# Optimization experiments

Measured on AMD Instinct MI355X. Metric: run time of the kernel, lower is better.

## Reference

```python
import jax, jax.numpy as jnp
import numpy as np

B, IN, OUT, TDIM, YDIM = 4096, 48, 64, 128, 64
HID = OUT * OUT  # 4096, Y_layer hidden/output width


def setup_inputs() -> dict:
    key = jax.random.key(0)
    ks = jax.random.split(key, 9)
    x = jax.random.normal(ks[0], (B, IN, IN), dtype=jnp.float32)
    # symmetrize so input is SPD-like (module assumes SPD inputs)
    x = 0.5 * (x + jnp.swapaxes(x, 1, 2))
    t = jax.random.normal(ks[1], (B, TDIM), dtype=jnp.float32)
    Y = jax.random.normal(ks[2], (B, YDIM), dtype=jnp.float32)
    # Stiefel (orthogonal) weight [input_size(=OUT after increase), output_size]
    W, _ = jnp.linalg.qr(jax.random.normal(ks[3], (OUT, OUT), dtype=jnp.float32))
    # Y_layer MLP params: Linear(YDIM,HID) -> SiLU -> Linear(HID,HID)
    Y_W1 = jax.random.normal(ks[4], (YDIM, HID), dtype=jnp.float32) / np.sqrt(YDIM)
    Y_b1 = jnp.zeros((HID,), dtype=jnp.float32)
    Y_W2 = jax.random.normal(ks[5], (HID, HID), dtype=jnp.float32) / np.sqrt(HID)
    Y_b2 = jnp.zeros((HID,), dtype=jnp.float32)
    return {"input": x, "t": t, "Y": Y, "W": W,
            "Y_W1": Y_W1, "Y_b1": Y_b1, "Y_W2": Y_W2, "Y_b2": Y_b2}


def reference(input, t, Y, W, Y_W1, Y_b1, Y_W2, Y_b2):
    # Y_layer MLP -> per-sample transform emb_Y [B, OUT, OUT]
    h = jax.nn.silu(Y @ Y_W1 + Y_b1)
    emb_Y = (h @ Y_W2 + Y_b2).reshape(B, OUT, OUT)
    # SPDIncreaseDim: embed input in top-left of OUTxOUT, ones on padded diagonal
    pad = OUT - IN
    xp = jnp.pad(input, ((0, 0), (0, pad), (0, pad)))
    add_diag = jnp.concatenate([jnp.zeros(IN, input.dtype), jnp.ones(pad, input.dtype)])
    xp = xp + jnp.diag(add_diag)[None]
    # congruence with Stiefel weight: W^T X W
    out = jnp.einsum('ji,bjk,kl->bil', W, xp, W)
    # congruence with MLP-generated weight: emb_Y X emb_Y^T
    out = jnp.einsum('bij,bjk,blk->bil', emb_Y, out, emb_Y)
    return out
```

## Files before the change

### kernel.cpp

```cpp
#include <hip/hip_runtime.h>
#include <hip/hip_bf16.h>

typedef __bf16 bf16;
typedef __bf16 bf16x8 __attribute__((ext_vector_type(8)));
typedef float floatx4 __attribute__((ext_vector_type(4)));

#define MFMA16(a, b, c) __builtin_amdgcn_mfma_f32_16x16x32_bf16((a), (b), (c), 0, 0, 0)

__device__ inline void gload_lds16(const void* g, void* l) {
    __builtin_amdgcn_global_load_lds((__attribute__((address_space(1))) void*)g,
                                     (__attribute__((address_space(3))) void*)l, 16, 0, 0);
}

__global__ __launch_bounds__(256) void prep_fused(
    const float* __restrict__ W2,
    const float* __restrict__ W,
    const float* __restrict__ b2,
    const float* __restrict__ Y,
    const float* __restrict__ W1,
    const float* __restrict__ b1,
    bf16* __restrict__ W2fT,
    float* __restrict__ b2f,
    bf16* __restrict__ h)
{
    __shared__ __align__(16) char smem[45056];
    int t = threadIdx.x, bid = blockIdx.x;
    int w = t >> 6, l = t & 63;
    int lm = l & 15, q2 = l >> 4, q8 = q2 * 8;

    if (bid < 2048) {
        int pt = bid & 31, i = bid >> 5;
        bf16* sW = (bf16*)smem;
        bf16* sA = sW + 64 * 72;
        bf16* sT = sA + 128 * 72;
        int p0 = pt * 128;

#pragma unroll
        for (int kk = 0; kk < 4; kk++) {
            int idx4 = t + 256 * kk;
            float4 v = *(const float4*)(W + (size_t)idx4 * 4);
            int row = (idx4 * 4) >> 6, col = (idx4 * 4) & 63;
            bf16 tmp[4] = {(bf16)v.x, (bf16)v.y, (bf16)v.z, (bf16)v.w};
            *(uint2*)(sW + row * 72 + col) = *(const uint2*)tmp;
        }
        {
            const float* src = W2 + (size_t)p0 * 4096 + i * 64;
#pragma unroll
            for (int kk = 0; kk < 8; kk++) {
                int c = t + 256 * kk;
                int row = c >> 4, j4 = (c & 15) * 4;
                float4 v = *(const float4*)(src + (size_t)row * 4096 + j4);
                bf16 tmp[4] = {(bf16)v.x, (bf16)v.y, (bf16)v.z, (bf16)v.w};
                *(uint2*)(sA + row * 72 + j4) = *(const uint2*)tmp;
            }
        }
        __syncthreads();

        floatx4 acc[2][4] = {};
#pragma unroll
        for (int kc = 0; kc < 2; kc++) {
            bf16x8 a0 = *(const bf16x8*)(sA + (w * 32 + lm) * 72 + kc * 32 + q8);
            bf16x8 a1 = *(const bf16x8*)(sA + (w * 32 + 16 + lm) * 72 + kc * 32 + q8);
#pragma unroll
            for (int jn = 0; jn < 4; jn++) {
                bf16x8 bf_ = *(const bf16x8*)(sW + (jn * 16 + lm) * 72 + kc * 32 + q8);
                acc[0][jn] = MFMA16(a0, bf_, acc[0][jn]);
                acc[1][jn] = MFMA16(a1, bf_, acc[1][jn]);
            }
        }
#pragma unroll
        for (int im = 0; im < 2; im++)
#pragma unroll
            for (int jn = 0; jn < 4; jn++) {
                int pr = w * 32 + im * 16 + q2 * 4;
                int lc = jn * 16 + lm;
                union { bf16 h4[4]; uint2 u; } pk;
#pragma unroll
                for (int r = 0; r < 4; r++) pk.h4[r] = (bf16)acc[im][jn][r];
                *(uint2*)(sT + lc * 136 + pr) = pk.u;
            }
        __syncthreads();
#pragma unroll
        for (int kk = 0; kk < 4; kk++) {
            int c = t + 256 * kk;
            int row = c >> 4, off = (c & 15) * 8;
            uint4 v = *(const uint4*)(sT + row * 136 + off);
            *(uint4*)(W2fT + (size_t)(i * 64 + row) * 4096 + p0 + off) = v;
        }
        return;
    }

    if (bid < 2112) {
        int i = bid - 2048;
        if (t < 64) {
            float acc = 0.f;
            const float* b2r = b2 + i * 64;
            const float* wr_ = W + t * 64;
#pragma unroll
            for (int j = 0; j < 64; j++) acc = fmaf(b2r[j], wr_[j], acc);
            b2f[i * 64 + t] = acc;
        }
        return;
    }

    {
        int q = bid - 2112;
        int m0 = (q >> 5) * 128, n0 = (q & 31) * 128;
        bf16* sY = (bf16*)smem;
        bf16* sWT = sY + 128 * 72;

#pragma unroll
        for (int kk = 0; kk < 8; kk++) {
            int c = t + 256 * kk;
            int row = c >> 4, c4 = (c & 15) * 4;
            float4 v = *(const float4*)(Y + (size_t)(m0 + row) * 64 + c4);
            bf16 tmp[4] = {(bf16)v.x, (bf16)v.y, (bf16)v.z, (bf16)v.w};
            *(uint2*)(sY + row * 72 + c4) = *(const uint2*)tmp;
        }
#pragma unroll
        for (int kk = 0; kk < 8; kk++) {
            int c = t + 256 * kk;
            int k = c >> 5, j4 = (c & 31) * 4;
            float4 v = *(const float4*)(W1 + (size_t)k * 4096 + n0 + j4);
            sWT[(j4 + 0) * 72 + k] = (bf16)v.x;
            sWT[(j4 + 1) * 72 + k] = (bf16)v.y;
            sWT[(j4 + 2) * 72 + k] = (bf16)v.z;
            sWT[(j4 + 3) * 72 + k] = (bf16)v.w;
        }
        __syncthreads();

        int wn = (w & 1) * 64, wm = (w >> 1) * 64;
        floatx4 acc[4][4] = {};
#pragma unroll
        for (int kc = 0; kc < 2; kc++) {
            bf16x8 af[4], bfr[4];
#pragma unroll
            for (int i = 0; i < 4; i++)
                af[i] = *(const bf16x8*)(sWT + (wn + i * 16 + lm) * 72 + kc * 32 + q8);
#pragma unroll
            for (int j = 0; j < 4; j++)
                bfr[j] = *(const bf16x8*)(sY + (wm + j * 16 + lm) * 72 + kc * 32 + q8);
#pragma unroll
            for (int i = 0; i < 4; i++)
#pragma unroll
                for (int j = 0; j < 4; j++)
                    acc[i][j] = MFMA16(af[i], bfr[j], acc[i][j]);
        }
#pragma unroll
        for (int i = 0; i < 4; i++) {
            int nb = n0 + wn + i * 16 + q2 * 4;
            float4 bv = *(const float4*)(b1 + nb);
            float bb[4] = {bv.x, bv.y, bv.z, bv.w};
#pragma unroll
            for (int j = 0; j < 4; j++) {
                int m = m0 + wm + j * 16 + lm;
                union { bf16 h4[4]; uint2 u; } pk;
#pragma unroll
                for (int r = 0; r < 4; r++) {
                    float v = acc[i][j][r] + bb[r];
                    v = v / (1.f + __expf(-v));
                    pk.h4[r] = (bf16)v;
                }
                *(uint2*)(h + (size_t)m * 4096 + nb) = pk.u;
            }
        }
    }
}

__global__ __launch_bounds__(512, 2) void gemm_bt_bias(
    const bf16* __restrict__ A, const bf16* __restrict__ BT,
    const float* __restrict__ bias, bf16* __restrict__ C,
    int M, int N, int K)
{
    __shared__ __align__(16) char lds[131072];

    int t = threadIdx.x, w = t >> 6, l = t & 63;
    int lm = l & 15, q2 = l >> 4;
    int wm = w >> 2, wn = w & 3;

    int bid = blockIdx.x;
    int xcd = bid & 7, local = bid >> 3;
    int m0 = ((xcd & 3) * 4 + (local >> 3)) * 256;
    int n0 = ((xcd >> 2) * 8 + (local & 7)) * 256;

    int c1 = t + 512;
    int ks0 = ((t & 3) ^ ((t >> 3) & 3)) * 8;
    int ks1 = ((c1 & 3) ^ ((c1 >> 3) & 3)) * 8;
    const bf16* gA0 = A + (size_t)(m0 + (t >> 2)) * K + ks0;
    const bf16* gA1 = A + (size_t)(m0 + (c1 >> 2)) * K + ks1;
    const bf16* gB0 = BT + (size_t)(n0 + (t >> 2)) * K + ks0;
    const bf16* gB1 = BT + (size_t)(n0 + (c1 >> 2)) * K + ks1;
    const int dst0 = (w * 64) * 16, dst1 = (512 + w * 64) * 16;

    auto issueA = [&](int slot) {
        char* slab = lds + slot * 32768;
        gload_lds16(gA0, slab + dst0);
        gload_lds16(gA1, slab + dst1);
        gA0 += 32; gA1 += 32;
    };
    auto issueB = [&](int slot) {
        char* slab = lds + slot * 32768;
        gload_lds16(gB0, slab + 16384 + dst0);
        gload_lds16(gB1, slab + 16384 + dst1);
        gB0 += 32; gB1 += 32;
    };

    const int qp16 = (q2 ^ ((lm >> 1) & 3)) * 16;
    const int aoff = (wm * 128 + lm) * 64 + qp16;
    const int boff = 16384 + (wn * 64 + lm) * 64 + qp16;

    floatx4 acc[8][4] = {};

    auto body = [&](int kt, bool doIssue) {
        const char* slab = lds + (kt & 3) * 32768;
        int s = (kt + 3) & 3;
        bf16x8 bv[4], a0[4], a1[4];
#pragma unroll
        for (int j = 0; j < 4; j++) bv[j] = *(const bf16x8*)(slab + boff + j * 1024);
#pragma unroll
        for (int i = 0; i < 4; i++) a0[i] = *(const bf16x8*)(slab + aoff + i * 1024);
        __builtin_amdgcn_sched_barrier(0);
#pragma unroll
        for (int i = 0; i < 4; i++) a1[i] = *(const bf16x8*)(slab + aoff + (4 + i) * 1024);
        if (doIssue) { issueA(s); issueB(s); }
        asm volatile("s_waitcnt lgkmcnt(4)" ::: "memory");
        __builtin_amdgcn_sched_barrier(0);
        __builtin_amdgcn_s_setprio(1);
#pragma unroll
        for (int i = 0; i < 4; i++)
#pragma unroll
            for (int j = 0; j < 4; j++) acc[i][j] = MFMA16(bv[j], a0[i], acc[i][j]);
        __builtin_amdgcn_s_setprio(0);
        asm volatile("s_waitcnt lgkmcnt(0)" ::: "memory");
        __builtin_amdgcn_sched_barrier(0);
        __builtin_amdgcn_s_setprio(1);
#pragma unroll
        for (int i = 0; i < 4; i++)
#pragma unroll
            for (int j = 0; j < 4; j++) acc[4 + i][j] = MFMA16(bv[j], a1[i], acc[4 + i][j]);
        __builtin_amdgcn_s_setprio(0);
        __builtin_amdgcn_sched_barrier(0);
    };

    issueA(0); issueB(0); issueA(1); issueB(1); issueA(2); issueB(2);
    asm volatile("s_waitcnt vmcnt(8)" ::: "memory");
    __builtin_amdgcn_s_barrier();
    const int KT = K >> 5;
    for (int kt = 0; kt < KT - 3; ++kt) {
        body(kt, true);
        asm volatile("s_waitcnt vmcnt(8)" ::: "memory");
        __builtin_amdgcn_s_barrier();
    }
    body(KT - 3, false);
    asm volatile("s_waitcnt vmcnt(4)" ::: "memory");
    __builtin_amdgcn_s_barrier();
    body(KT - 2, false);
    asm volatile("s_waitcnt vmcnt(0)" ::: "memory");
    __builtin_amdgcn_s_barrier();
    body(KT - 1, false);

#pragma unroll
    for (int i = 0; i < 8; i++) {
        int m = m0 + wm * 128 + i * 16 + lm;
#pragma unroll
        for (int j = 0; j < 4; j++) {
            int nb = n0 + wn * 64 + j * 16 + q2 * 4;
            float4 b4 = *(const float4*)(bias + nb);
            float bb[4] = {b4.x, b4.y, b4.z, b4.w};
            union { bf16 h4[4]; uint2 u; } pk;
#pragma unroll
            for (int r = 0; r < 4; r++) pk.h4[r] = (bf16)(acc[i][j][r] + bb[r]);
            *(uint2*)(C + (size_t)m * N + nb) = pk.u;
        }
    }
}

#define ST 72
__global__ __launch_bounds__(256) void batched_congruence(
    const float* __restrict__ x,
    const bf16* __restrict__ F,
    float* __restrict__ out)
{
    __shared__ bf16 sX[64 * ST], sF[64 * ST], sT[64 * ST];
    int t = threadIdx.x, w = t >> 6, l = t & 63;
    int b = blockIdx.x;
    int lm = l & 15, q2 = l >> 4, q8 = q2 * 8;
    int r0 = (w >> 1) * 32, c0 = (w & 1) * 32;

    const float4* xb = (const float4*)(x + (size_t)b * 2304);
    float4 v0 = xb[t];
    float4 v1 = xb[t + 256];
    float4 v2 = (t < 64) ? xb[t + 512] : make_float4(0.f, 0.f, 0.f, 0.f);

    {
        const uint4* gf = (const uint4*)(F + (size_t)b * 4096);
#pragma unroll
        for (int kk = 0; kk < 2; kk++) {
            int c = t + 256 * kk;
            *(uint4*)(sF + (c >> 3) * ST + (c & 7) * 8) = gf[c];
        }
    }
    {
        unsigned* sx32 = (unsigned*)sX;
#pragma unroll
        for (int kk = 0; kk < 4; kk++) {
            int idx = t + 256 * kk;
            if (idx < 384) {
                int r = idx >> 3, d = 24 + (idx & 7);
                sx32[r * 36 + d] = 0u;
            } else if (idx < 896) {
                int k2 = idx - 384;
                int r = 48 + (k2 >> 5), d = k2 & 31;
                unsigned val = 0u;
                if (d == (r >> 1)) val = (r & 1) ? 0x3F800000u : 0x00003F80u;
                sx32[r * 36 + d] = val;
            }
        }
    }
    {
        int c = t;
        bf16 p4[4];
        p4[0] = (bf16)v0.x; p4[1] = (bf16)v0.y; p4[2] = (bf16)v0.z; p4[3] = (bf16)v0.w;
        *(uint2*)(sX + (c / 12) * ST + (c % 12) * 4) = *(const uint2*)p4;
        c = t + 256;
        p4[0] = (bf16)v1.x; p4[1] = (bf16)v1.y; p4[2] = (bf16)v1.z; p4[3] = (bf16)v1.w;
        *(uint2*)(sX + (c / 12) * ST + (c % 12) * 4) = *(const uint2*)p4;
        if (t < 64) {
            c = t + 512;
            p4[0] = (bf16)v2.x; p4[1] = (bf16)v2.y; p4[2] = (bf16)v2.z; p4[3] = (bf16)v2.w;
            *(uint2*)(sX + (c / 12) * ST + (c % 12) * 4) = *(const uint2*)p4;
        }
    }
    __syncthreads();

    auto mm = [&](const bf16* PA, const bf16* PB, floatx4 acc[2][2]) {
#pragma unroll
        for (int kc = 0; kc < 2; kc++) {
            bf16x8 a0 = *(const bf16x8*)(PA + (r0 + lm) * ST + kc * 32 + q8);
            bf16x8 a1 = *(const bf16x8*)(PA + (r0 + 16 + lm) * ST + kc * 32 + q8);
            bf16x8 b0 = *(const bf16x8*)(PB + (c0 + lm) * ST + kc * 32 + q8);
            bf16x8 b1 = *(const bf16x8*)(PB + (c0 + 16 + lm) * ST + kc * 32 + q8);
            acc[0][0] = MFMA16(a0, b0, acc[0][0]);
            acc[0][1] = MFMA16(a0, b1, acc[0][1]);
            acc[1][0] = MFMA16(a1, b0, acc[1][0]);
            acc[1][1] = MFMA16(a1, b1, acc[1][1]);
        }
    };

    floatx4 z = {0.f, 0.f, 0.f, 0.f};
    {
        floatx4 acc[2][2] = {{z, z}, {z, z}};
        mm(sX, sF, acc);
#pragma unroll
        for (int i = 0; i < 2; i++)
#pragma unroll
            for (int j = 0; j < 2; j++) {
                int R = r0 + i * 16 + q2 * 4;
                int Cc = c0 + j * 16 + lm;
                union { bf16 h4[4]; uint2 u; } pk;
#pragma unroll
                for (int r = 0; r < 4; r++) pk.h4[r] = (bf16)acc[i][j][r];
                *(uint2*)(sT + Cc * ST + R) = pk.u;
            }
    }
    __syncthreads();
    {
        floatx4 acc[2][2] = {{z, z}, {z, z}};
        mm(sT, sF, acc);
        float* stage = (float*)sX;
        float* ob = out + (size_t)b * 4096;
        if (w < 2) {
#pragma unroll
            for (int i = 0; i < 2; i++)
#pragma unroll
                for (int j = 0; j < 2; j++) {
                    int R = r0 + i * 16 + q2 * 4;
                    int Cc = c0 + j * 16 + lm;
#pragma unroll
                    for (int r = 0; r < 4; r++) stage[(R + r) * 64 + Cc] = acc[i][j][r];
                }
        }
        __syncthreads();
#pragma unroll
        for (int kk = 0; kk < 2; kk++) {
            int idx = t + 256 * kk;
            *(float4*)(ob + (size_t)idx * 4) = *(const float4*)(stage + (size_t)idx * 4);
        }
        __syncthreads();
        if (w >= 2) {
#pragma unroll
            for (int i = 0; i < 2; i++)
#pragma unroll
                for (int j = 0; j < 2; j++) {
                    int R = r0 + i * 16 + q2 * 4 - 32;
                    int Cc = c0 + j * 16 + lm;
#pragma unroll
                    for (int r = 0; r < 4; r++) stage[(R + r) * 64 + Cc] = acc[i][j][r];
                }
        }
        __syncthreads();
#pragma unroll
        for (int kk = 0; kk < 2; kk++) {
            int idx = t + 256 * kk;
            *(float4*)(ob + 2048 + (size_t)idx * 4) = *(const float4*)(stage + (size_t)idx * 4);
        }
    }
}

extern "C" void kernel_launch(void* const* d_in, const int* in_sizes, int n_in,
                              void* d_out, int out_size, void* d_ws, size_t ws_size,
                              hipStream_t stream) {
    const float* x  = (const float*)d_in[0];
    const float* Y  = (const float*)d_in[2];
    const float* W  = (const float*)d_in[3];
    const float* W1 = (const float*)d_in[4];
    const float* b1 = (const float*)d_in[5];
    const float* W2 = (const float*)d_in[6];
    const float* b2 = (const float*)d_in[7];
    float* out = (float*)d_out;

    const size_t NN = (size_t)4096 * 4096;
    bf16* h    = (bf16*)d_ws;
    bf16* W2fT = h + NN;
    bf16* emb  = W2fT + NN;
    float* b2f = (float*)d_out;

    prep_fused<<<3136, 256, 0, stream>>>(W2, W, b2, Y, W1, b1, W2fT, b2f, h);
    gemm_bt_bias<<<256, 512, 0, stream>>>(h, W2fT, b2f, emb, 4096, 4096, 4096);
    batched_congruence<<<4096, 256, 0, stream>>>(x, emb, out);
}
```

Before: 307.5 us.

## Switch GEMM pipeline to double-buffered BK=64 slabs with one barrier per step

```diff
diff --git a/kernel.cpp b/kernel.cpp
--- a/kernel.cpp
+++ b/kernel.cpp
@@ -183,46 +183,51 @@
     int m0 = ((xcd & 3) * 4 + (local >> 3)) * 256;
     int n0 = ((xcd >> 2) * 8 + (local & 7)) * 256;
 
-    int c1 = t + 512;
-    int ks0 = ((t & 3) ^ ((t >> 3) & 3)) * 8;
-    int ks1 = ((c1 & 3) ^ ((c1 >> 3) & 3)) * 8;
-    const bf16* gA0 = A + (size_t)(m0 + (t >> 2)) * K + ks0;
-    const bf16* gA1 = A + (size_t)(m0 + (c1 >> 2)) * K + ks1;
-    const bf16* gB0 = BT + (size_t)(n0 + (t >> 2)) * K + ks0;
-    const bf16* gB1 = BT + (size_t)(n0 + (c1 >> 2)) * K + ks1;
-    const int dst0 = (w * 64) * 16, dst1 = (512 + w * 64) * 16;
-
-    auto issueA = [&](int slot) {
-        char* slab = lds + slot * 32768;
-        gload_lds16(gA0, slab + dst0);
-        gload_lds16(gA1, slab + dst1);
-        gA0 += 32; gA1 += 32;
+    const bf16 *gA0, *gA1, *gA2, *gA3, *gB0, *gB1, *gB2, *gB3;
+    {
+        int ch, row, ko;
+        ch = t;        row = ch >> 3; ko = ((ch & 7) ^ (row & 7)) * 8;
+        gA0 = A + (size_t)(m0 + row) * K + ko; gB0 = BT + (size_t)(n0 + row) * K + ko;
+        ch = t + 512;  row = ch >> 3; ko = ((ch & 7) ^ (row & 7)) * 8;
+        gA1 = A + (size_t)(m0 + row) * K + ko; gB1 = BT + (size_t)(n0 + row) * K + ko;
+        ch = t + 1024; row = ch >> 3; ko = ((ch & 7) ^ (row & 7)) * 8;
+        gA2 = A + (size_t)(m0 + row) * K + ko; gB2 = BT + (size_t)(n0 + row) * K + ko;
+        ch = t + 1536; row = ch >> 3; ko = ((ch & 7) ^ (row & 7)) * 8;
+        gA3 = A + (size_t)(m0 + row) * K + ko; gB3 = BT + (size_t)(n0 + row) * K + ko;
+    }
+    const int dstb = t * 16;
+
+    auto issue = [&](int slot) {
+        char* slab = lds + (slot << 16);
+        gload_lds16(gA0, slab + dstb);
+        gload_lds16(gA1, slab + 8192 + dstb);
+        gload_lds16(gA2, slab + 16384 + dstb);
+        gload_lds16(gA3, slab + 24576 + dstb);
+        gload_lds16(gB0, slab + 32768 + dstb);
+        gload_lds16(gB1, slab + 40960 + dstb);
+        gload_lds16(gB2, slab + 49152 + dstb);
+        gload_lds16(gB3, slab + 57344 + dstb);
+        gA0 += 64; gA1 += 64; gA2 += 64; gA3 += 64;
+        gB0 += 64; gB1 += 64; gB2 += 64; gB3 += 64;
     };
-    auto issueB = [&](int slot) {
-        char* slab = lds + slot * 32768;
-        gload_lds16(gB0, slab + 16384 + dst0);
-        gload_lds16(gB1, slab + 16384 + dst1);
-        gB0 += 32; gB1 += 32;
-    };
-
-    const int qp16 = (q2 ^ ((lm >> 1) & 3)) * 16;
-    const int aoff = (wm * 128 + lm) * 64 + qp16;
-    const int boff = 16384 + (wn * 64 + lm) * 64 + qp16;
+
+    const int swz = (q2 ^ (lm & 7)) * 16;
+    const int base_a = (wm * 128 + lm) * 128 + swz;
+    const int base_b = 32768 + (wn * 64 + lm) * 128 + swz;
 
     floatx4 acc[8][4] = {};
 
     auto body = [&](int kt, bool doIssue) {
-        const char* slab = lds + (kt & 3) * 32768;
-        int s = (kt + 3) & 3;
+        const char* slab = lds + ((kt & 1) << 16);
         bf16x8 bv[4], a0[4], a1[4];
 #pragma unroll
-        for (int j = 0; j < 4; j++) bv[j] = *(const bf16x8*)(slab + boff + j * 1024);
-#pragma unroll
-        for (int i = 0; i < 4; i++) a0[i] = *(const bf16x8*)(slab + aoff + i * 1024);
-        __builtin_amdgcn_sched_barrier(0);
-#pragma unroll
-        for (int i = 0; i < 4; i++) a1[i] = *(const bf16x8*)(slab + aoff + (4 + i) * 1024);
-        if (doIssue) { issueA(s); issueB(s); }
+        for (int j = 0; j < 4; j++) bv[j] = *(const bf16x8*)(slab + base_b + j * 2048);
+#pragma unroll
+        for (int i = 0; i < 4; i++) a0[i] = *(const bf16x8*)(slab + base_a + i * 2048);
+        __builtin_amdgcn_sched_barrier(0);
+#pragma unroll
+        for (int i = 0; i < 4; i++) a1[i] = *(const bf16x8*)(slab + base_a + (4 + i) * 2048);
+        if (doIssue) issue((kt + 1) & 1);
         asm volatile("s_waitcnt lgkmcnt(4)" ::: "memory");
         __builtin_amdgcn_sched_barrier(0);
         __builtin_amdgcn_s_setprio(1);
@@ -240,24 +245,43 @@
             for (int j = 0; j < 4; j++) acc[4 + i][j] = MFMA16(bv[j], a1[i], acc[4 + i][j]);
         __builtin_amdgcn_s_setprio(0);
         __builtin_amdgcn_sched_barrier(0);
+#pragma unroll
+        for (int j = 0; j < 4; j++) bv[j] = *(const bf16x8*)(slab + (base_b ^ 64) + j * 2048);
+#pragma unroll
+        for (int i = 0; i < 4; i++) a0[i] = *(const bf16x8*)(slab + (base_a ^ 64) + i * 2048);
+        __builtin_amdgcn_sched_barrier(0);
+#pragma unroll
+        for (int i = 0; i < 4; i++) a1[i] = *(const bf16x8*)(slab + (base_a ^ 64) + (4 + i) * 2048);
+        asm volatile("s_waitcnt lgkmcnt(4)" ::: "memory");
+        __builtin_amdgcn_sched_barrier(0);
+        __builtin_amdgcn_s_setprio(1);
+#pragma unroll
+        for (int i = 0; i < 4; i++)
+#pragma unroll
+            for (int j = 0; j < 4; j++) acc[i][j] = MFMA16(bv[j], a0[i], acc[i][j]);
+        __builtin_amdgcn_s_setprio(0);
+        asm volatile("s_waitcnt lgkmcnt(0)" ::: "memory");
+        __builtin_amdgcn_sched_barrier(0);
+        __builtin_amdgcn_s_setprio(1);
+#pragma unroll
+        for (int i = 0; i < 4; i++)
+#pragma unroll
+            for (int j = 0; j < 4; j++) acc[4 + i][j] = MFMA16(bv[j], a1[i], acc[4 + i][j]);
+        __builtin_amdgcn_s_setprio(0);
+        __builtin_amdgcn_sched_barrier(0);
+        if (doIssue) {
+            asm volatile("s_waitcnt vmcnt(0)" ::: "memory");
+            __builtin_amdgcn_s_barrier();
+            __builtin_amdgcn_sched_barrier(0);
+        }
     };
 
-    issueA(0); issueB(0); issueA(1); issueB(1); issueA(2); issueB(2);
-    asm volatile("s_waitcnt vmcnt(8)" ::: "memory");
-    __builtin_amdgcn_s_barrier();
-    const int KT = K >> 5;
-    for (int kt = 0; kt < KT - 3; ++kt) {
-        body(kt, true);
-        asm volatile("s_waitcnt vmcnt(8)" ::: "memory");
-        __builtin_amdgcn_s_barrier();
-    }
-    body(KT - 3, false);
-    asm volatile("s_waitcnt vmcnt(4)" ::: "memory");
-    __builtin_amdgcn_s_barrier();
-    body(KT - 2, false);
+    issue(0);
     asm volatile("s_waitcnt vmcnt(0)" ::: "memory");
     __builtin_amdgcn_s_barrier();
-    body(KT - 1, false);
+    __builtin_amdgcn_sched_barrier(0);
+    const int KT = K >> 6;
+    for (int kt = 0; kt < KT; ++kt) body(kt, kt + 1 < KT);
 
 #pragma unroll
     for (int i = 0; i < 8; i++) {
```

Measured after the change: 297.9 us. 1.03x faster.
